# Kernel optimization log

Hardware: AMD Instinct MI355X
Metric: run time of the kernel (lower is better)

## Reference

```python
import jax, jax.numpy as jnp
import numpy as np

N_NODES = 50000
N_COMS = 4
E = 800000
IN_DIM = 128
COM_DIM = 32  # emb_dim 128 split across 4 communities
BN_EPS = 1e-5


def _gin_layer(h, src, dst, ew, W1, b1, W2, b2, gamma, beta):
    # GINConv (eps=0): out = MLP(h + sum_{j->i} ew_j * h_j)
    msg = h[src] * ew[:, None]                      # [E, F]
    aggr = jax.ops.segment_sum(msg, dst, num_segments=N_NODES)
    z = h + aggr
    z = jax.nn.relu(z @ W1 + b1) @ W2 + b2          # Linear-ReLU-Linear MLP
    # BatchNorm1d (training mode: batch statistics), then ReLU. dropout p=0.
    mu = z.mean(axis=0)
    var = z.var(axis=0)
    z = (z - mu) * jax.lax.rsqrt(var + BN_EPS) * gamma + beta
    return jax.nn.relu(z)


def setup_inputs() -> dict:
    key = jax.random.key(0)
    ks = jax.random.split(key, 12)
    d = {
        'x': jax.random.normal(ks[0], (N_NODES, IN_DIM), jnp.float32),
        'edge_index': jax.random.randint(ks[1], (2, E), 0, N_NODES, jnp.int32),
        'edge_weights': jax.random.uniform(ks[2], (N_COMS, E), jnp.float32),
        'l0_W1': jax.random.normal(ks[3], (IN_DIM, COM_DIM), jnp.float32) * 0.05,
        'l0_b1': jnp.zeros((COM_DIM,), jnp.float32),
        'l0_W2': jax.random.normal(ks[4], (COM_DIM, COM_DIM), jnp.float32) * 0.05,
        'l0_b2': jnp.zeros((COM_DIM,), jnp.float32),
        'l0_gamma': jnp.ones((COM_DIM,), jnp.float32),
        'l0_beta': jnp.zeros((COM_DIM,), jnp.float32),
        'l1_W1': jax.random.normal(ks[5], (COM_DIM, COM_DIM), jnp.float32) * 0.05,
        'l1_b1': jnp.zeros((COM_DIM,), jnp.float32),
        'l1_W2': jax.random.normal(ks[6], (COM_DIM, COM_DIM), jnp.float32) * 0.05,
        'l1_b2': jnp.zeros((COM_DIM,), jnp.float32),
        'l1_gamma': jnp.ones((COM_DIM,), jnp.float32),
        'l1_beta': jnp.zeros((COM_DIM,), jnp.float32),
        'enc_W': jax.random.normal(ks[7], (IN_DIM, IN_DIM), jnp.float32) * 0.05,
        'enc_b': jnp.zeros((IN_DIM,), jnp.float32),
    }
    return d


def reference(x, edge_index, edge_weights,
              l0_W1, l0_b1, l0_W2, l0_b2, l0_gamma, l0_beta,
              l1_W1, l1_b1, l1_W2, l1_b2, l1_gamma, l1_beta,
              enc_W, enc_b):
    src, dst = edge_index[0], edge_index[1]
    layer_params = [
        (l0_W1, l0_b1, l0_W2, l0_b2, l0_gamma, l0_beta),
        (l1_W1, l1_b1, l1_W2, l1_b2, l1_gamma, l1_beta),
    ]
    # Shared ComGNN applied with each community's edge weights.
    per_com = []  # per_com[k] = list of N_layers outputs [N, COM_DIM]
    for k in range(N_COMS):
        h = x
        hs = []
        for p in layer_params:
            h = _gin_layer(h, src, dst, edge_weights[k], *p)
            hs.append(h)
        per_com.append(hs)
    # zip over layers, concat over communities -> [N, emb_dim]
    layer_outs = [jnp.concatenate([per_com[k][i] for k in range(N_COMS)], axis=-1)
                  for i in range(len(layer_params))]
    out0 = x @ enc_W + enc_b  # input_encoder(x)
    return jnp.stack([out0] + layer_outs)  # [1+N_layers, N, emb_dim]
```

## Files before the change

kernel.cpp:

```cpp
#include <hip/hip_runtime.h>
#include <hip/hip_bf16.h>
#include <math.h>

#define NN 50000
#define NE 800000
#define NK 4
#define FD 128
#define CD 32
#define CAP 48
#define BNCH 1000
#define BNROWS 50
#define NRANGE 6250

typedef unsigned short u16;

__device__ __forceinline__ u16 f2bf(float x) {
    union { float f; unsigned u; } c; c.f = x;
    unsigned r = c.u + 0x7fffu + ((c.u >> 16) & 1u);
    return (u16)(r >> 16);
}
__device__ __forceinline__ float bflo(unsigned pair) {
    union { unsigned u; float f; } c; c.u = pair << 16;
    return c.f;
}
__device__ __forceinline__ float bfhi(unsigned pair) {
    union { unsigned u; float f; } c; c.u = pair & 0xffff0000u;
    return c.f;
}


__global__ void k_scatter(const int* __restrict__ src, const int* __restrict__ dst,
                          const float* __restrict__ ew,
                          int* __restrict__ cnt, int4* __restrict__ sse) {
    int xcd = blockIdx.x & 7;
    int e = (blockIdx.x >> 3) * 256 + threadIdx.x;
    int d = dst[e];
    int lo = xcd * NRANGE;
    if ((unsigned)(d - lo) < (unsigned)NRANGE) {
        int p = atomicAdd(&cnt[d], 1);
        unsigned w01 = (unsigned)f2bf(ew[e]) | ((unsigned)f2bf(ew[(size_t)NE + e]) << 16);
        unsigned w23 = (unsigned)f2bf(ew[(size_t)2 * NE + e]) | ((unsigned)f2bf(ew[(size_t)3 * NE + e]) << 16);
        sse[(size_t)d * CAP + p] = make_int4(src[e], (int)w01, (int)w23, 0);
    }
}


__global__ void __launch_bounds__(256) k_enc_y0(const float* __restrict__ x,
                                                const float* __restrict__ W,
                                                const float* __restrict__ b,
                                                const float* __restrict__ W1,
                                                float* __restrict__ out,
                                                u16* __restrict__ y0) {
    __shared__ float xsT[FD][68];
    int tid = threadIdx.x;
    int nbase = blockIdx.x * 64;

    int r = tid >> 2;
    int cg = (tid & 3) * 32;
    int gn = nbase + r;
    const float* xr = x + (size_t)(gn < NN ? gn : NN - 1) * FD;
#pragma unroll
    for (int q = 0; q < 8; ++q) {
        float4 v = *(const float4*)(xr + cg + q * 4);
        int f = cg + q * 4;
        xsT[f][r] = v.x; xsT[f + 1][r] = v.y; xsT[f + 2][r] = v.z; xsT[f + 3][r] = v.w;
    }
    __syncthreads();

    int cq = (tid & 31) * 4;
    int col = tid & 31;
    int g = tid >> 5;
    float acc[8][4];
    float acy[8];
#pragma unroll
    for (int i = 0; i < 8; ++i) {
        acy[i] = 0.f;
#pragma unroll
        for (int j = 0; j < 4; ++j) acc[i][j] = 0.f;
    }

    for (int f = 0; f < FD; ++f) {
        float4 wv = *(const float4*)(W + f * FD + cq);
        float w1 = W1[f * CD + col];
        float4 xa = *(const float4*)&xsT[f][g * 8];
        float4 xb = *(const float4*)&xsT[f][g * 8 + 4];
        float xn[8] = {xa.x, xa.y, xa.z, xa.w, xb.x, xb.y, xb.z, xb.w};
#pragma unroll
        for (int i = 0; i < 8; ++i) {
            acc[i][0] += xn[i] * wv.x;
            acc[i][1] += xn[i] * wv.y;
            acc[i][2] += xn[i] * wv.z;
            acc[i][3] += xn[i] * wv.w;
            acy[i] += xn[i] * w1;
        }
    }
    float4 bv = *(const float4*)(b + cq);
#pragma unroll
    for (int i = 0; i < 8; ++i) {
        int n = nbase + g * 8 + i;
        if (n < NN) {
            float4 o;
            o.x = acc[i][0] + bv.x;
            o.y = acc[i][1] + bv.y;
            o.z = acc[i][2] + bv.z;
            o.w = acc[i][3] + bv.w;
            *(float4*)(out + (size_t)n * FD + cq) = o;
            y0[(size_t)n * CD + col] = f2bf(acy[i]);
        }
    }
}


template <int STRIDE>
__global__ void __launch_bounds__(256) k_aggr(const u16* __restrict__ y,
                                              const int* __restrict__ cnt,
                                              const int4* __restrict__ sse,
                                              const float* __restrict__ b1,
                                              const float* __restrict__ W2,
                                              const float* __restrict__ b2,
                                              float* __restrict__ u) {
    __shared__ float W2s[CD][CD];
    __shared__ float b2s[CD];
    __shared__ float tls[4][NK][36];
    int tid = threadIdx.x;
    for (int i = tid; i < CD * CD; i += 256) W2s[i >> 5][i & 31] = W2[i];
    if (tid < CD) b2s[tid] = b2[tid];
    __syncthreads();

    int w = tid >> 6;
    int lane = tid & 63;
    int hi = lane >> 5;
    int sub = lane & 31;
    int k = sub >> 3;
    int fq = sub & 7;
    int f0 = fq * 4;
    int col = (STRIDE == CD) ? f0 : (k * CD + f0);
    const u16* yb = y + col;
    bool klow = k < 2;
    int lsh = (k & 1) ? 0 : 16;

    int nbase0 = blockIdx.x * 16 + w * 4;
    int4 c4 = *(const int4*)(cnt + nbase0);
    int cdeg[4] = {c4.x, c4.y, c4.z, c4.w};

    float4 bv = *(const float4*)(b1 + f0);
    float4 b2v = *(const float4*)&b2s[f0];

#pragma unroll 1
    for (int it = 0; it < 4; ++it) {
        int node = nbase0 + it;
        int beg = node * CAP;
        int end = beg + cdeg[it];

        float a0 = 0.f, a1 = 0.f, a2 = 0.f, a3 = 0.f;
        for (int j0 = beg; j0 < end; j0 += 8) {
            int ssv[4];
            float wwv[4];
#pragma unroll
            for (int q = 0; q < 4; ++q) {
                int jj = j0 + q * 2 + hi;
                bool ok = jj < end;
                int jc = ok ? jj : beg;
                int4 ee = sse[jc];
                ssv[q] = ee.x;
                unsigned wp = klow ? (unsigned)ee.y : (unsigned)ee.z;
                unsigned wb = (wp << lsh) & 0xffff0000u;
                union { unsigned u; float f; } cv; cv.u = wb;
                wwv[q] = ok ? cv.f : 0.f;
            }
#pragma unroll
            for (int q = 0; q < 4; ++q) {
                uint2 pv = *(const uint2*)(yb + (size_t)ssv[q] * STRIDE);
                float wq = wwv[q];
                a0 += wq * bflo(pv.x);
                a1 += wq * bfhi(pv.x);
                a2 += wq * bflo(pv.y);
                a3 += wq * bfhi(pv.y);
            }
        }
        a0 += __shfl_xor(a0, 32);
        a1 += __shfl_xor(a1, 32);
        a2 += __shfl_xor(a2, 32);
        a3 += __shfl_xor(a3, 32);

        uint2 hv = *(const uint2*)(yb + (size_t)node * STRIDE);
        float t0 = fmaxf(bflo(hv.x) + a0 + bv.x, 0.f);
        float t1 = fmaxf(bfhi(hv.x) + a1 + bv.y, 0.f);
        float t2 = fmaxf(bflo(hv.y) + a2 + bv.z, 0.f);
        float t3 = fmaxf(bfhi(hv.y) + a3 + bv.w, 0.f);
        if (hi == 0) {
            float4 tv = {t0, t1, t2, t3};
            *(float4*)&tls[w][k][f0] = tv;
        }
        __threadfence_block();

        int m0 = hi * 16;
        float c0 = 0.f, c1 = 0.f, c2 = 0.f, c3 = 0.f;
#pragma unroll
        for (int mm = 0; mm < 16; ++mm) {
            float tm = tls[w][k][m0 + mm];
            float4 wv = *(const float4*)&W2s[m0 + mm][f0];
            c0 += tm * wv.x;
            c1 += tm * wv.y;
            c2 += tm * wv.z;
            c3 += tm * wv.w;
        }
        c0 += __shfl_xor(c0, 32);
        c1 += __shfl_xor(c1, 32);
        c2 += __shfl_xor(c2, 32);
        c3 += __shfl_xor(c3, 32);
        if (hi == 0) {
            float4 o = {c0 + b2v.x, c1 + b2v.y, c2 + b2v.z, c3 + b2v.w};
            *(float4*)(u + (size_t)node * FD + k * CD + f0) = o;
        }
        __threadfence_block();
    }
}


__global__ void __launch_bounds__(256) k_bn_stats1(const float* __restrict__ u,
                                                   float* __restrict__ part) {
    int ch = blockIdx.x;
    int c = threadIdx.x & 127;
    int rg = threadIdx.x >> 7;
    float s1 = 0.f, s2 = 0.f;
    int nend = (ch + 1) * BNROWS;
    for (int n = ch * BNROWS + rg; n < nend; n += 2) {
        float v = u[(size_t)n * FD + c];
        s1 += v;
        s2 += v * v;
    }
    __shared__ float sh1[2][FD], sh2[2][FD];
    sh1[rg][c] = s1;
    sh2[rg][c] = s2;
    __syncthreads();
    if (rg == 0) {
        s1 += sh1[1][c];
        s2 += sh2[1][c];
        float2 p = {s1, s2};
        *(float2*)(part + ((size_t)ch * FD + c) * 2) = p;
    }
}

__global__ void __launch_bounds__(256) k_bn_stats2(const float* __restrict__ part,
                                                   const float* __restrict__ gamma,
                                                   const float* __restrict__ beta,
                                                   float* __restrict__ bnp) {
    int c = blockIdx.x;
    int tid = threadIdx.x;
    float S1 = 0.f, S2 = 0.f;
    for (int ch = tid; ch < BNCH; ch += 256) {
        float2 p = *(const float2*)(part + ((size_t)ch * FD + c) * 2);
        S1 += p.x;
        S2 += p.y;
    }
    __shared__ float sh1[256], sh2[256];
    sh1[tid] = S1;
    sh2[tid] = S2;
    __syncthreads();
    for (int off = 128; off > 0; off >>= 1) {
        if (tid < off) {
            sh1[tid] += sh1[tid + off];
            sh2[tid] += sh2[tid + off];
        }
        __syncthreads();
    }
    if (tid == 0) {
        float mean = sh1[0] / (float)NN;
        float var = sh2[0] / (float)NN - mean * mean;
        int f = c & 31;
        float scale = gamma[f] * rsqrtf(var + 1e-5f);
        bnp[c * 2] = scale;
        bnp[c * 2 + 1] = beta[f] - mean * scale;
    }
}


__global__ void __launch_bounds__(256) k_bn_y1(const float* __restrict__ uu,
                                               const float* __restrict__ bnp,
                                               const float* __restrict__ W1,
                                               float* __restrict__ plane,
                                               u16* __restrict__ y1) {
    __shared__ float W1s[CD][CD];
    __shared__ float bnsp[NK][68];
    int tid = threadIdx.x;
    for (int i = tid; i < CD * CD; i += 256) W1s[i >> 5][i & 31] = W1[i];
    bnsp[tid >> 6][tid & 63] = bnp[tid & 255];
    __syncthreads();

    int gid = blockIdx.x * 256 + tid;
    int node = gid >> 5;
    int sub = gid & 31;
    int k = sub >> 3;
    int j4 = (sub & 7) * 4;

    const float* ur = uu + (size_t)node * FD + k * CD;
    float acc0 = 0.f, acc1 = 0.f, acc2 = 0.f, acc3 = 0.f;
#pragma unroll
    for (int q = 0; q < 8; ++q) {
        float4 uv = *(const float4*)(ur + q * 4);
        float4 p0 = *(const float4*)&bnsp[k][q * 8];
        float4 p1 = *(const float4*)&bnsp[k][q * 8 + 4];
        float h0 = fmaxf(fmaf(uv.x, p0.x, p0.y), 0.f);
        float h1 = fmaxf(fmaf(uv.y, p0.z, p0.w), 0.f);
        float h2 = fmaxf(fmaf(uv.z, p1.x, p1.y), 0.f);
        float h3 = fmaxf(fmaf(uv.w, p1.z, p1.w), 0.f);
        float4 w0 = *(const float4*)&W1s[q * 4 + 0][j4];
        float4 w1 = *(const float4*)&W1s[q * 4 + 1][j4];
        float4 w2 = *(const float4*)&W1s[q * 4 + 2][j4];
        float4 w3 = *(const float4*)&W1s[q * 4 + 3][j4];
        acc0 += h0 * w0.x + h1 * w1.x + h2 * w2.x + h3 * w3.x;
        acc1 += h0 * w0.y + h1 * w1.y + h2 * w2.y + h3 * w3.y;
        acc2 += h0 * w0.z + h1 * w1.z + h2 * w2.z + h3 * w3.z;
        acc3 += h0 * w0.w + h1 * w1.w + h2 * w2.w + h3 * w3.w;
    }
    float4 uo = *(const float4*)(uu + (size_t)node * FD + sub * 4);
    float4 q0 = *(const float4*)&bnsp[k][(sub & 7) * 8];
    float4 q1 = *(const float4*)&bnsp[k][(sub & 7) * 8 + 4];
    float4 po;
    po.x = fmaxf(fmaf(uo.x, q0.x, q0.y), 0.f);
    po.y = fmaxf(fmaf(uo.y, q0.z, q0.w), 0.f);
    po.z = fmaxf(fmaf(uo.z, q1.x, q1.y), 0.f);
    po.w = fmaxf(fmaf(uo.w, q1.z, q1.w), 0.f);
    *(float4*)(plane + (size_t)node * FD + sub * 4) = po;

    uint2 pk;
    pk.x = (unsigned)f2bf(acc0) | ((unsigned)f2bf(acc1) << 16);
    pk.y = (unsigned)f2bf(acc2) | ((unsigned)f2bf(acc3) << 16);
    *(uint2*)(y1 + (size_t)node * FD + sub * 4) = pk;
}


__global__ void __launch_bounds__(256) k_bn_apply(const float* __restrict__ u,
                                                  const float* __restrict__ bnp,
                                                  float* __restrict__ out) {
    int gid = blockIdx.x * 256 + threadIdx.x;
    int c0 = (gid & 31) * 4;
    float4 v = *(const float4*)(u + (size_t)gid * 4);
    float4 s0 = *(const float4*)(bnp + c0 * 2);
    float4 s1 = *(const float4*)(bnp + c0 * 2 + 4);
    float4 o;
    o.x = fmaxf(fmaf(v.x, s0.x, s0.y), 0.f);
    o.y = fmaxf(fmaf(v.y, s0.z, s0.w), 0.f);
    o.z = fmaxf(fmaf(v.z, s1.x, s1.y), 0.f);
    o.w = fmaxf(fmaf(v.w, s1.z, s1.w), 0.f);
    *(float4*)(out + (size_t)gid * 4) = o;
}


extern "C" void kernel_launch(void* const* d_in, const int* in_sizes, int n_in,
                              void* d_out, int out_size, void* d_ws, size_t ws_size,
                              hipStream_t stream) {
    const float* x = (const float*)d_in[0];
    const int* ei = (const int*)d_in[1];
    const float* ew = (const float*)d_in[2];
    const float* l0W1 = (const float*)d_in[3];
    const float* l0b1 = (const float*)d_in[4];
    const float* l0W2 = (const float*)d_in[5];
    const float* l0b2 = (const float*)d_in[6];
    const float* l0g = (const float*)d_in[7];
    const float* l0be = (const float*)d_in[8];
    const float* l1W1 = (const float*)d_in[9];
    const float* l1b1 = (const float*)d_in[10];
    const float* l1W2 = (const float*)d_in[11];
    const float* l1b2 = (const float*)d_in[12];
    const float* l1g = (const float*)d_in[13];
    const float* l1be = (const float*)d_in[14];
    const float* encW = (const float*)d_in[15];
    const float* encb = (const float*)d_in[16];
    float* out = (float*)d_out;

    char* ws = (char*)d_ws;
    size_t off = 0;
    auto alloc = [&](size_t bytes) -> void* {
        void* p = ws + off;
        off += (bytes + 255) & ~(size_t)255;
        return p;
    };
    int* dcnt = (int*)alloc((size_t)NN * 4);
    int4* dsse = (int4*)alloc((size_t)NN * CAP * 16);
    u16* dy0 = (u16*)alloc((size_t)NN * CD * 2);
    u16* dy1 = (u16*)alloc((size_t)NN * FD * 2);
    float* du = (float*)alloc((size_t)NN * FD * 4);
    float* dpart = (float*)alloc((size_t)BNCH * FD * 2 * 4);
    float* dbnp = (float*)alloc((size_t)FD * 2 * 4);

    const int* src = ei;
    const int* dst = ei + NE;

    hipMemsetAsync(dcnt, 0, (size_t)NN * 4, stream);
    k_scatter<<<(NE / 256) * 8, 256, 0, stream>>>(src, dst, ew, dcnt, dsse);
    k_enc_y0<<<(NN + 63) / 64, 256, 0, stream>>>(x, encW, encb, l0W1, out, dy0);

    float* plane1 = out + (size_t)NN * FD;
    k_aggr<CD><<<NN / 16, 256, 0, stream>>>(dy0, dcnt, dsse, l0b1, l0W2, l0b2, du);
    k_bn_stats1<<<BNCH, 256, 0, stream>>>(du, dpart);
    k_bn_stats2<<<FD, 256, 0, stream>>>(dpart, l0g, l0be, dbnp);
    k_bn_y1<<<NN * 32 / 256, 256, 0, stream>>>(du, dbnp, l1W1, plane1, dy1);

    float* plane2 = out + (size_t)2 * NN * FD;
    k_aggr<FD><<<NN / 16, 256, 0, stream>>>(dy1, dcnt, dsse, l1b1, l1W2, l1b2, du);
    k_bn_stats1<<<BNCH, 256, 0, stream>>>(du, dpart);
    k_bn_stats2<<<FD, 256, 0, stream>>>(dpart, l1g, l1be, dbnp);
    k_bn_apply<<<NN * 32 / 256, 256, 0, stream>>>(du, dbnp, plane2);
}
```

Baseline: 225.7 us.

## Fuse BatchNorm partial statistics into aggregation kernel and widen edge unroll

Each aggregation block now accumulates per-channel sum and sum-of-squares of its outputs and writes per-block partials, removing the separate stats pass that re-read the full 50000x128 float buffer twice per forward. The second-stage reduction now sums over 3125 partials instead of 1000, so it does more work. The edge-gather loop also processes 16 edges per iteration instead of 8, putting more loads in flight at the cost of extra registers and more masked work for low-degree nodes.

```diff
diff --git a/kernel.cpp b/kernel.cpp
--- a/kernel.cpp
+++ b/kernel.cpp
@@ -8,8 +8,7 @@
 #define FD 128
 #define CD 32
 #define CAP 48
-#define BNCH 1000
-#define BNROWS 50
+#define MBLK 3125
 #define NRANGE 6250
 
 typedef unsigned short u16;
@@ -118,10 +117,12 @@
                                               const float* __restrict__ b1,
                                               const float* __restrict__ W2,
                                               const float* __restrict__ b2,
-                                              float* __restrict__ u) {
+                                              float* __restrict__ u,
+                                              float* __restrict__ part) {
     __shared__ float W2s[CD][CD];
     __shared__ float b2s[CD];
     __shared__ float tls[4][NK][36];
+    __shared__ float shs1[4][32][4], shs2[4][32][4];
     int tid = threadIdx.x;
     for (int i = tid; i < CD * CD; i += 256) W2s[i >> 5][i & 31] = W2[i];
     if (tid < CD) b2s[tid] = b2[tid];
@@ -145,6 +146,8 @@
 
     float4 bv = *(const float4*)(b1 + f0);
     float4 b2v = *(const float4*)&b2s[f0];
+    float s10 = 0.f, s11 = 0.f, s12 = 0.f, s13 = 0.f;
+    float s20 = 0.f, s21 = 0.f, s22 = 0.f, s23 = 0.f;
 
 #pragma unroll 1
     for (int it = 0; it < 4; ++it) {
@@ -153,11 +156,11 @@
         int end = beg + cdeg[it];
 
         float a0 = 0.f, a1 = 0.f, a2 = 0.f, a3 = 0.f;
-        for (int j0 = beg; j0 < end; j0 += 8) {
-            int ssv[4];
-            float wwv[4];
-#pragma unroll
-            for (int q = 0; q < 4; ++q) {
+        for (int j0 = beg; j0 < end; j0 += 16) {
+            int ssv[8];
+            float wwv[8];
+#pragma unroll
+            for (int q = 0; q < 8; ++q) {
                 int jj = j0 + q * 2 + hi;
                 bool ok = jj < end;
                 int jc = ok ? jj : beg;
@@ -169,7 +172,7 @@
                 wwv[q] = ok ? cv.f : 0.f;
             }
 #pragma unroll
-            for (int q = 0; q < 4; ++q) {
+            for (int q = 0; q < 8; ++q) {
                 uint2 pv = *(const uint2*)(yb + (size_t)ssv[q] * STRIDE);
                 float wq = wwv[q];
                 a0 += wq * bflo(pv.x);
@@ -210,37 +213,42 @@
         c2 += __shfl_xor(c2, 32);
         c3 += __shfl_xor(c3, 32);
         if (hi == 0) {
-            float4 o = {c0 + b2v.x, c1 + b2v.y, c2 + b2v.z, c3 + b2v.w};
+            float o0 = c0 + b2v.x, o1 = c1 + b2v.y, o2 = c2 + b2v.z, o3 = c3 + b2v.w;
+            float4 o = {o0, o1, o2, o3};
             *(float4*)(u + (size_t)node * FD + k * CD + f0) = o;
+            s10 += o0; s20 += o0 * o0;
+            s11 += o1; s21 += o1 * o1;
+            s12 += o2; s22 += o2 * o2;
+            s13 += o3; s23 += o3 * o3;
         }
         __threadfence_block();
     }
-}
-
-
-__global__ void __launch_bounds__(256) k_bn_stats1(const float* __restrict__ u,
-                                                   float* __restrict__ part) {
-    int ch = blockIdx.x;
-    int c = threadIdx.x & 127;
-    int rg = threadIdx.x >> 7;
-    float s1 = 0.f, s2 = 0.f;
-    int nend = (ch + 1) * BNROWS;
-    for (int n = ch * BNROWS + rg; n < nend; n += 2) {
-        float v = u[(size_t)n * FD + c];
-        s1 += v;
-        s2 += v * v;
-    }
-    __shared__ float sh1[2][FD], sh2[2][FD];
-    sh1[rg][c] = s1;
-    sh2[rg][c] = s2;
+
+    if (hi == 0) {
+        float4 v1 = {s10, s11, s12, s13};
+        float4 v2 = {s20, s21, s22, s23};
+        *(float4*)&shs1[w][sub][0] = v1;
+        *(float4*)&shs2[w][sub][0] = v2;
+    }
     __syncthreads();
-    if (rg == 0) {
-        s1 += sh1[1][c];
-        s2 += sh2[1][c];
-        float2 p = {s1, s2};
-        *(float2*)(part + ((size_t)ch * FD + c) * 2) = p;
-    }
-}
+    if (tid < 32) {
+        float S1[4] = {0.f, 0.f, 0.f, 0.f}, S2[4] = {0.f, 0.f, 0.f, 0.f};
+#pragma unroll
+        for (int ww = 0; ww < 4; ++ww) {
+            float4 v1 = *(const float4*)&shs1[ww][tid][0];
+            float4 v2 = *(const float4*)&shs2[ww][tid][0];
+            S1[0] += v1.x; S1[1] += v1.y; S1[2] += v1.z; S1[3] += v1.w;
+            S2[0] += v2.x; S2[1] += v2.y; S2[2] += v2.z; S2[3] += v2.w;
+        }
+        int c0 = (tid >> 3) * CD + (tid & 7) * 4;
+#pragma unroll
+        for (int j = 0; j < 4; ++j) {
+            float2 p = {S1[j], S2[j]};
+            *(float2*)(part + ((size_t)blockIdx.x * FD + c0 + j) * 2) = p;
+        }
+    }
+}
+
 
 __global__ void __launch_bounds__(256) k_bn_stats2(const float* __restrict__ part,
                                                    const float* __restrict__ gamma,
@@ -249,7 +257,7 @@
     int c = blockIdx.x;
     int tid = threadIdx.x;
     float S1 = 0.f, S2 = 0.f;
-    for (int ch = tid; ch < BNCH; ch += 256) {
+    for (int ch = tid; ch < MBLK; ch += 256) {
         float2 p = *(const float2*)(part + ((size_t)ch * FD + c) * 2);
         S1 += p.x;
         S2 += p.y;
@@ -382,7 +390,7 @@
     u16* dy0 = (u16*)alloc((size_t)NN * CD * 2);
     u16* dy1 = (u16*)alloc((size_t)NN * FD * 2);
     float* du = (float*)alloc((size_t)NN * FD * 4);
-    float* dpart = (float*)alloc((size_t)BNCH * FD * 2 * 4);
+    float* dpart = (float*)alloc((size_t)MBLK * FD * 2 * 4);
     float* dbnp = (float*)alloc((size_t)FD * 2 * 4);
 
     const int* src = ei;
@@ -393,14 +401,12 @@
     k_enc_y0<<<(NN + 63) / 64, 256, 0, stream>>>(x, encW, encb, l0W1, out, dy0);
 
     float* plane1 = out + (size_t)NN * FD;
-    k_aggr<CD><<<NN / 16, 256, 0, stream>>>(dy0, dcnt, dsse, l0b1, l0W2, l0b2, du);
-    k_bn_stats1<<<BNCH, 256, 0, stream>>>(du, dpart);
+    k_aggr<CD><<<MBLK, 256, 0, stream>>>(dy0, dcnt, dsse, l0b1, l0W2, l0b2, du, dpart);
     k_bn_stats2<<<FD, 256, 0, stream>>>(dpart, l0g, l0be, dbnp);
     k_bn_y1<<<NN * 32 / 256, 256, 0, stream>>>(du, dbnp, l1W1, plane1, dy1);
 
     float* plane2 = out + (size_t)2 * NN * FD;
-    k_aggr<FD><<<NN / 16, 256, 0, stream>>>(dy1, dcnt, dsse, l1b1, l1W2, l1b2, du);
-    k_bn_stats1<<<BNCH, 256, 0, stream>>>(du, dpart);
+    k_aggr<FD><<<MBLK, 256, 0, stream>>>(dy1, dcnt, dsse, l1b1, l1W2, l1b2, du, dpart);
     k_bn_stats2<<<FD, 256, 0, stream>>>(dpart, l1g, l1be, dbnp);
     k_bn_apply<<<NN * 32 / 256, 256, 0, stream>>>(du, dbnp, plane2);
 }
```

Result: no change. 227.7 us (+0.9%).
